# Kernel tuning notes

Hardware: AMD Instinct MI355X
Metric: run time of the kernel (lower is better)

Reference implementation:

```python
import jax, jax.numpy as jnp
import numpy as np

N_QUBITS = 8
N_LAYERS = 4
N_WIRES = N_QUBITS + 1  # circuit uses an extra ancilla wire
B = 16384
D = 512
LN_EPS = 1e-5


def _rx(theta):
    # RX(t) = [[cos(t/2), -i sin(t/2)], [-i sin(t/2), cos(t/2)]]; theta: () or (B,)
    c = jnp.cos(theta / 2).astype(jnp.complex64)
    s = (-1j) * jnp.sin(theta / 2).astype(jnp.complex64)
    return jnp.stack([jnp.stack([c, s], -1), jnp.stack([s, c], -1)], -2)


def _ry(theta):
    c = jnp.cos(theta / 2).astype(jnp.complex64)
    s = jnp.sin(theta / 2).astype(jnp.complex64)
    return jnp.stack([jnp.stack([c, -s], -1), jnp.stack([s, c], -1)], -2)


def _rz(theta):
    # RZ(t) = diag(e^{-it/2}, e^{it/2})
    half = (theta / 2).astype(jnp.complex64)
    em = jnp.exp(-1j * half)
    ep = jnp.exp(1j * half)
    z = jnp.zeros_like(em)
    return jnp.stack([jnp.stack([em, z], -1), jnp.stack([z, ep], -1)], -2)


def _apply_1q(state, U, wire):
    # state: (B,) + (2,)*N_WIRES ; U: (2,2) shared or (B,2,2) per-sample
    ax = 1 + wire
    s = jnp.moveaxis(state, ax, -1)
    if U.ndim == 2:
        s = jnp.einsum('ij,...j->...i', U, s)
    else:
        s = jnp.einsum('bij,b...j->b...i', U, s)
    return jnp.moveaxis(s, -1, ax)


def _cnot(state, c, t):
    # flip target wire t on the control=1 slice of wire c
    s = jnp.moveaxis(state, (1 + c, 1 + t), (-2, -1))
    s = jnp.stack([s[..., 0, :], jnp.flip(s[..., 1, :], axis=-1)], axis=-2)
    return jnp.moveaxis(s, (-2, -1), (1 + c, 1 + t))


def _quantum_circuit(angles, q_weights):
    # angles: (B, N_QUBITS) per-sample data angles; q_weights: (N_LAYERS, N_QUBITS+1)
    b = angles.shape[0]
    state = jnp.zeros((b, 2 ** N_WIRES), jnp.complex64).at[:, 0].set(1.0)
    state = state.reshape((b,) + (2,) * N_WIRES)
    # data encoding: RX, RZ with per-sample angles
    for i in range(N_QUBITS):
        state = _apply_1q(state, _rx(angles[:, i]), i)
        state = _apply_1q(state, _rz(angles[:, i]), i)
    # first variational layer
    for i in range(N_QUBITS):
        state = _apply_1q(state, _rx(q_weights[0, i]), i)
        state = _apply_1q(state, _rz(q_weights[1, i]), i)
    # entangling layers
    for l in range(1, N_LAYERS):
        for i in range(N_QUBITS):
            state = _cnot(state, i, (i + 1) % N_QUBITS)
            state = _apply_1q(state, _ry(q_weights[l, i]), i)
            state = _apply_1q(state, _rz(q_weights[l, i]), i)
        state = _cnot(state, N_QUBITS - 1, N_QUBITS)
        state = _apply_1q(state, _ry(q_weights[l, -1]), N_QUBITS)
    probs = state.real ** 2 + state.imag ** 2
    # <Z_i> = P(q_i=0) - P(q_i=1)
    zs = []
    for i in range(N_QUBITS):
        axes = tuple(1 + j for j in range(N_WIRES) if j != i)
        p = probs.sum(axes)  # (B, 2)
        zs.append(p[:, 0] - p[:, 1])
    return jnp.stack(zs, axis=1)  # (B, N_QUBITS)


def _forward(x, timestep, w_in, b_in, ln_gamma, ln_beta, q_weights, w_out, b_out):
    h = jnp.tanh(x @ w_in.T + b_in)  # (B, 8)
    mu = h.mean(-1, keepdims=True)
    var = ((h - mu) ** 2).mean(-1, keepdims=True)
    h = (h - mu) / jnp.sqrt(var + LN_EPS) * ln_gamma + ln_beta
    angles = h + timestep  # broadcast scalar timestep
    q_out = _quantum_circuit(angles, q_weights)
    out = q_out @ w_out.T + b_out
    return x + out  # input_dim == output_dim -> residual


def setup_inputs() -> dict:
    key = jax.random.key(0)
    ks = jax.random.split(key, 6)
    x = jax.random.normal(ks[0], (B, D), jnp.float32)
    timestep = jax.random.uniform(ks[1], (1,), jnp.float32)
    w_in = jax.random.normal(ks[2], (N_QUBITS, D), jnp.float32) * np.float32(1.0 / np.sqrt(D))
    b_in = jnp.zeros((N_QUBITS,), jnp.float32)
    ln_gamma = jnp.ones((N_QUBITS,), jnp.float32)
    ln_beta = jnp.zeros((N_QUBITS,), jnp.float32)
    q_weights = jax.random.uniform(ks[3], (N_LAYERS, N_QUBITS + 1), jnp.float32, 0.0, 2.0 * np.pi)
    w_out = jax.random.normal(ks[4], (D, N_QUBITS), jnp.float32) * np.float32(1.0 / np.sqrt(N_QUBITS))
    b_out = jnp.zeros((D,), jnp.float32)
    return {'x': x, 'timestep': timestep, 'w_in': w_in, 'b_in': b_in,
            'ln_gamma': ln_gamma, 'ln_beta': ln_beta, 'q_weights': q_weights,
            'w_out': w_out, 'b_out': b_out}


def reference(x, timestep, w_in, b_in, ln_gamma, ln_beta, q_weights, w_out, b_out):
    return _forward(x, timestep, w_in, b_in, ln_gamma, ln_beta, q_weights, w_out, b_out)
```

## Files before the change

### kernel.cpp

```cpp
#include <hip/hip_runtime.h>
#include <math.h>

#define NSAMP 16384
#define ND    512

typedef float f2 __attribute__((ext_vector_type(2)));
__device__ __forceinline__ f2 spl(float x) { return (f2){x, x}; }

template<int CTRL>
__device__ __forceinline__ float dppf(float x) {
  return __int_as_float(__builtin_amdgcn_update_dpp(
      __float_as_int(x), __float_as_int(x), CTRL, 0xF, 0xF, true));
}
template<int CTRL, int RM, int BM>
__device__ __forceinline__ float dppf_keep(float x) {
  return __int_as_float(__builtin_amdgcn_update_dpp(
      __float_as_int(x), __float_as_int(x), CTRL, RM, BM, false));
}
template<int P>
__device__ __forceinline__ float swzf(float x) {
  return __int_as_float(__builtin_amdgcn_ds_swizzle(__float_as_int(x), P));
}
__device__ __forceinline__ float bpermf(int addrB, float x) {
  return __int_as_float(__builtin_amdgcn_ds_bpermute(addrB, __float_as_int(x)));
}

#if __has_builtin(__builtin_amdgcn_permlane16_swap)
#define HAVE_PLSWAP 1
#endif
__device__ __forceinline__ void plswap16(float x, float& a, float& b) {
#ifdef HAVE_PLSWAP
  auto r = __builtin_amdgcn_permlane16_swap(__float_as_uint(x), __float_as_uint(x), false, false);
  a = __uint_as_float(r[0]); b = __uint_as_float(r[1]);
#else
  a = x; b = swzf<0x401F>(x);
#endif
}
__device__ __forceinline__ void plswap32(float x, float& a, float& b) {
#ifdef HAVE_PLSWAP
  auto r = __builtin_amdgcn_permlane32_swap(__float_as_uint(x), __float_as_uint(x), false, false);
  a = __uint_as_float(r[0]); b = __uint_as_float(r[1]);
#else
  a = x; b = __shfl_xor(x, 32, 64);
#endif
}

template<int M>
__device__ __forceinline__ f2 bfly2(f2 x) {
  f2 r;
  if constexpr (M == 1)       { r.x = dppf<0xB1>(x.x);    r.y = dppf<0xB1>(x.y); }
  else if constexpr (M == 2)  { r.x = dppf<0x4E>(x.x);    r.y = dppf<0x4E>(x.y); }
  else if constexpr (M == 8)  { r.x = dppf<0x128>(x.x);   r.y = dppf<0x128>(x.y); }
  else if constexpr (M == 4)  { r.x = swzf<0x101F>(x.x);  r.y = swzf<0x101F>(x.y); }
  else if constexpr (M == 16) { r.x = swzf<0x401F>(x.x);  r.y = swzf<0x401F>(x.y); }
  else                        { r.x = __shfl_xor(x.x, 32, 64); r.y = __shfl_xor(x.y, 32, 64); }
  return r;
}

__device__ __forceinline__ void fold8_allsum2(const float* yA, const float* yB,
                                              int lane, float& rA, float& rB) {
  float a4[4], b4[4];
#pragma unroll
  for (int i = 0; i < 4; ++i) {
    float kA = (lane & 1) ? yA[2 * i + 1] : yA[2 * i];
    float sA = (lane & 1) ? yA[2 * i]     : yA[2 * i + 1];
    float kB = (lane & 1) ? yB[2 * i + 1] : yB[2 * i];
    float sB = (lane & 1) ? yB[2 * i]     : yB[2 * i + 1];
    a4[i] = kA + dppf<0xB1>(sA);
    b4[i] = kB + dppf<0xB1>(sB);
  }
  float a2[2], b2[2];
#pragma unroll
  for (int i = 0; i < 2; ++i) {
    float kA = (lane & 2) ? a4[2 * i + 1] : a4[2 * i];
    float sA = (lane & 2) ? a4[2 * i]     : a4[2 * i + 1];
    float kB = (lane & 2) ? b4[2 * i + 1] : b4[2 * i];
    float sB = (lane & 2) ? b4[2 * i]     : b4[2 * i + 1];
    a2[i] = kA + dppf<0x4E>(sA);
    b2[i] = kB + dppf<0x4E>(sB);
  }
  float kA = (lane & 4) ? a2[1] : a2[0];
  float sA = (lane & 4) ? a2[0] : a2[1];
  float kB = (lane & 4) ? b2[1] : b2[0];
  float sB = (lane & 4) ? b2[0] : b2[1];
  rA = kA + swzf<0x101F>(sA);
  rB = kB + swzf<0x101F>(sB);
  rA += dppf<0x128>(rA);
  rB += dppf<0x128>(rB);
  { float a, b; plswap16(rA, a, b); rA = a + b; }
  { float a, b; plswap16(rB, a, b); rB = a + b; }
  { float a, b; plswap32(rA, a, b); rA = a + b; }
  { float a, b; plswap32(rB, a, b); rB = a + b; }
}

__device__ __forceinline__ float grp8_sum(float x) {
  x += dppf<0xB1>(x);
  x += dppf<0x4E>(x);
  x += swzf<0x101F>(x);
  return x;
}

__device__ __forceinline__ f2 cmul(f2 a, f2 b) {
  f2 bs = __builtin_shufflevector(b, b, 1, 0);
  f2 t  = (f2){-a.y, a.y} * bs;
  return spl(a.x) * b + t;
}

template<int LB>
__device__ __forceinline__ void ry_local(f2* s, float c, float sv) {
#pragma unroll
  for (int r0 = 0; r0 < 16; ++r0) {
    if ((r0 & 7) & (1 << LB)) continue;
    const int r1 = r0 | (1 << LB);
    f2 a0 = s[r0], a1 = s[r1];
    s[r0] = spl(c) * a0 - spl(sv) * a1;
    s[r1] = spl(sv) * a0 + spl(c) * a1;
  }
}
template<int LB>
__device__ __forceinline__ void rz_local(f2* s, f2 phm, f2 php) {
#pragma unroll
  for (int r = 0; r < 16; ++r) s[r] = cmul(s[r], ((r & 7) & (1 << LB)) ? php : phm);
}
template<int M>
__device__ __forceinline__ void ry_lane(f2* s, float c, float se) {
#pragma unroll
  for (int r = 0; r < 16; ++r) {
    f2 p = bfly2<M>(s[r]);
    s[r] = spl(c) * s[r] + spl(se) * p;
  }
}
template<int CB, int TB>
__device__ __forceinline__ void cnot_ll(f2* s) {
#pragma unroll
  for (int r0 = 0; r0 < 16; ++r0) {
    if (!((r0 & 7) & (1 << CB)) || ((r0 & 7) & (1 << TB))) continue;
    const int r1 = r0 | (1 << TB);
    f2 t = s[r0]; s[r0] = s[r1]; s[r1] = t;
  }
}
template<int CB, int TM>
__device__ __forceinline__ void cnot_lt(f2* s) {
#pragma unroll
  for (int r = 0; r < 16; ++r) {
    if (!((r & 7) & (1 << CB))) continue;
    s[r] = bfly2<TM>(s[r]);
  }
}
__device__ __forceinline__ void cnot_bperm(f2* s, int addrB) {
#pragma unroll
  for (int r = 0; r < 16; ++r) {
    s[r].x = bpermf(addrB, s[r].x);
    s[r].y = bpermf(addrB, s[r].y);
  }
}
__device__ __forceinline__ void cnot_m4_t1(f2* s) {
#pragma unroll
  for (int r = 0; r < 16; ++r) {
    s[r].x = dppf_keep<0xB1, 0xF, 0xA>(s[r].x);
    s[r].y = dppf_keep<0xB1, 0xF, 0xA>(s[r].y);
  }
}
__device__ __forceinline__ void cnot_m1_t2(f2* s) {
#pragma unroll
  for (int r = 0; r < 16; ++r) {
    s[r].x = dppf<0x6C>(s[r].x);
    s[r].y = dppf<0x6C>(s[r].y);
  }
}
template<int TB>
__device__ __forceinline__ void cnot_tl(f2* s, bool cc) {
#pragma unroll
  for (int r0 = 0; r0 < 16; ++r0) {
    if ((r0 & 7) & (1 << TB)) continue;
    const int r1 = r0 | (1 << TB);
    f2 n0, n1;
    n0.x = cc ? s[r1].x : s[r0].x;  n0.y = cc ? s[r1].y : s[r0].y;
    n1.x = cc ? s[r0].x : s[r1].x;  n1.y = cc ? s[r0].y : s[r1].y;
    s[r0] = n0; s[r1] = n1;
  }
}

__global__ void qpre_kernel(const float* __restrict__ qw, float* __restrict__ ws) {
  int t = threadIdx.x;
  if (t < 27) {
    float s, c; __sincosf(qw[9 + t] * 0.5f, &s, &c);
    ws[2 * t] = c; ws[2 * t + 1] = s;
  }
}

template<bool PRE>
struct Consts {
  const float* qw; const float* ws;
  __device__ __forceinline__ f2 ltrig(int l, int i) const {
    if constexpr (PRE) {
      return ((const f2*)ws)[(l - 1) * 9 + i];
    } else {
      float s, c; __sincosf(qw[l * 9 + i] * 0.5f, &s, &c);
      return (f2){c, s};
    }
  }
};

template<bool PRE, int MODE>
__device__ __forceinline__ void do_layer(f2* st, int lane, const Consts<PRE>& cst, int l,
                                         int addr56, int addr67, int addr78) {
  f2 t[9];
#pragma unroll
  for (int i = 0; i < 9; ++i) t[i] = cst.ltrig(l, i);

  cnot_ll<0, 1>(st);
  ry_local<0>(st, t[0].x, t[0].y);
  rz_local<0>(st, (f2){t[0].x, -t[0].y}, (f2){t[0].x, t[0].y});
  cnot_ll<1, 2>(st);
  ry_local<1>(st, t[1].x, t[1].y);
  cnot_lt<2, 4>(st);
  ry_local<2>(st, t[2].x, t[2].y);
  cnot_m4_t1(st);
  { float se = (lane & 4) ? t[3].y : -t[3].y;
    ry_lane<4>(st, t[3].x, se); }
  cnot_m1_t2(st);
  { float se = (lane & 1) ? t[4].y : -t[4].y;
    ry_lane<1>(st, t[4].x, se); }
  cnot_bperm(st, addr56);
  { float se = (lane & 2) ? t[5].y : -t[5].y;
    ry_lane<2>(st, t[5].x, se); }
  cnot_bperm(st, addr67);
  { float se = (lane & 8) ? t[6].y : -t[6].y;
    ry_lane<8>(st, t[6].x, se); }
  cnot_tl<0>(st, (lane & 16) != 0);
  { float se = (lane & 16) ? t[7].y : -t[7].y;
    ry_lane<16>(st, t[7].x, se); }

  if constexpr (MODE == 1) {
    const float wsel = (lane & 32) ? ((lane & 16) ? t[8].x : t[8].y)
                                   : ((lane & 16) ? -t[8].y : t[8].x);
#pragma unroll
    for (int r = 0; r < 16; ++r) st[r] = st[r] * spl(wsel);
  }
  if constexpr (MODE == 2) {
    cnot_bperm(st, addr78);
  }
  if constexpr (MODE != 3) {
    f2 L4[4];
#pragma unroll
    for (int k = 0; k < 4; ++k) {
      f2 p1 = (f2){t[1].x, (k & 1) ? t[1].y : -t[1].y};
      f2 p2 = (f2){t[2].x, (k & 2) ? t[2].y : -t[2].y};
      L4[k] = cmul(p1, p2);
    }
    f2 phW = (f2){t[3].x, (lane & 4)  ? t[3].y : -t[3].y};
    phW = cmul(phW, (f2){t[4].x, (lane & 1)  ? t[4].y : -t[4].y});
    phW = cmul(phW, (f2){t[5].x, (lane & 2)  ? t[5].y : -t[5].y});
    phW = cmul(phW, (f2){t[6].x, (lane & 8)  ? t[6].y : -t[6].y});
    phW = cmul(phW, (f2){t[7].x, (lane & 16) ? t[7].y : -t[7].y});
    f2 pr[4];
#pragma unroll
    for (int k = 0; k < 4; ++k) pr[k] = cmul(L4[k], phW);
#pragma unroll
    for (int r = 0; r < 16; ++r) st[r] = cmul(st[r], pr[((r & 7) >> 1) & 3]);
  }
}

template<bool PRE>
__global__ __launch_bounds__(256, 4) void qlayer_kernel(
    const float* __restrict__ x, const float* __restrict__ tstep,
    const float* __restrict__ w_in, const float* __restrict__ b_in,
    const float* __restrict__ g, const float* __restrict__ be,
    const float* __restrict__ qw, const float* __restrict__ w_out,
    const float* __restrict__ b_out, float* __restrict__ out,
    const float* __restrict__ ws)
{
  __shared__ __align__(16) float s_u[4][2][8][4];
  __shared__ __align__(16) float s_z[4][2][8];

  const int tid    = threadIdx.x;
  const int lane   = tid & 63;
  const int wv     = tid >> 6;
  const int smpA   = blockIdx.x * 8 + wv * 2;
  const int smpB   = smpA + 1;
  const int jq     = lane & 7;
  const int dbase  = lane << 3;

  const int addr56 = (lane ^ ((lane & 2) << 2)) << 2;
  const int addr67 = (lane ^ ((lane & 8) << 1)) << 2;
  const int addr78 = (lane ^ ((lane & 16) << 1)) << 2;

  const float4* xrA = (const float4*)(x + (size_t)smpA * ND + dbase);
  const float4* xrB = (const float4*)(x + (size_t)smpB * ND + dbase);
  const float4 xaA = xrA[0], xbA = xrA[1];
  const float4 xaB = xrB[0], xbB = xrB[1];
  const f2 a0 = (f2){xaA.x, xaA.y}, a1 = (f2){xaA.z, xaA.w};
  const f2 a2 = (f2){xbA.x, xbA.y}, a3 = (f2){xbA.z, xbA.w};
  const f2 b0 = (f2){xaB.x, xaB.y}, b1 = (f2){xaB.z, xaB.w};
  const f2 b2 = (f2){xbB.x, xbB.y}, b3 = (f2){xbB.z, xbB.w};

  float hA[8], hB[8];
#pragma unroll
  for (int j = 0; j < 8; ++j) {
    const float4* wj = (const float4*)(w_in + j * ND + dbase);
    float4 wa = wj[0], wb = wj[1];
    f2 w0 = (f2){wa.x, wa.y}, w1 = (f2){wa.z, wa.w};
    f2 w2 = (f2){wb.x, wb.y}, w3 = (f2){wb.z, wb.w};
    f2 accA = a0 * w0 + a1 * w1 + a2 * w2 + a3 * w3;
    f2 accB = b0 * w0 + b1 * w1 + b2 * w2 + b3 * w3;
    hA[j] = accA.x + accA.y;
    hB[j] = accB.x + accB.y;
  }
  float HA, HB;
  fold8_allsum2(hA, hB, lane, HA, HB);

  const float t0  = tstep[0];
  const float bj  = b_in[jq];
  const float gj  = g[jq];
  const float bej = be[jq];
  float tjA, tjB;
  {
    float vA = fminf(15.f, fmaxf(-15.f, HA + bj));
    float vB = fminf(15.f, fmaxf(-15.f, HB + bj));
    float eA = __expf(2.f * vA), eB = __expf(2.f * vB);
    tjA = (eA - 1.f) * __builtin_amdgcn_rcpf(eA + 1.f);
    tjB = (eB - 1.f) * __builtin_amdgcn_rcpf(eB + 1.f);
  }
  const float muA = grp8_sum(tjA) * 0.125f;
  const float muB = grp8_sum(tjB) * 0.125f;
  const float dvA = tjA - muA, dvB = tjB - muB;
  const float varA = grp8_sum(dvA * dvA) * 0.125f;
  const float varB = grp8_sum(dvB * dvB) * 0.125f;
  const float angA = dvA * rsqrtf(varA + 1e-5f) * gj + bej + t0;
  const float angB = dvB * rsqrtf(varB + 1e-5f) * gj + bej + t0;

  {
    float s0, c0, s1, c1;
    __sincosf(qw[jq] * 0.5f, &s0, &c0);
    __sincosf(qw[9 + jq] * 0.5f, &s1, &c1);
    f2 M00 = (f2){ c1 * c0, -s1 * c0};
    f2 M01 = (f2){-s1 * s0, -c1 * s0};
    f2 M10 = (f2){ s1 * s0, -c1 * s0};
    f2 M11 = (f2){ c1 * c0,  s1 * c0};
    float saA, caA; __sincosf(angA * 0.5f, &saA, &caA);
    float saB, caB; __sincosf(angB * 0.5f, &saB, &caB);
    f2 v0A = spl(caA) * (f2){caA, -saA};
    f2 v1A = spl(saA) * (f2){saA, -caA};
    f2 v0B = spl(caB) * (f2){caB, -saB};
    f2 v1B = spl(saB) * (f2){saB, -caB};
    f2 u0A = cmul(M00, v0A) + cmul(M01, v1A);
    f2 u1A = cmul(M10, v0A) + cmul(M11, v1A);
    f2 u0B = cmul(M00, v0B) + cmul(M01, v1B);
    f2 u1B = cmul(M10, v0B) + cmul(M11, v1B);
    if (lane < 16) {
      const int sb = lane >> 3;
      f2 u0 = sb ? u0B : u0A;
      f2 u1 = sb ? u1B : u1A;
      *(float4*)&s_u[wv][sb][jq][0] = (float4){u0.x, u0.y, u1.x, u1.y};
    }
  }
  asm volatile("s_waitcnt lgkmcnt(0)" ::: "memory");
  __builtin_amdgcn_sched_barrier(0);

  f2 st[16];
#pragma unroll
  for (int smp = 0; smp < 2; ++smp) {
    const f2* ub = (const f2*)&s_u[wv][smp][0][0];
    f2 r4 = ub[4 * 2 + ((lane >> 0) & 1)];
    f2 r5 = ub[5 * 2 + ((lane >> 1) & 1)];
    f2 r3 = ub[3 * 2 + ((lane >> 2) & 1)];
    f2 r6 = ub[6 * 2 + ((lane >> 3) & 1)];
    f2 r7 = ub[7 * 2 + ((lane >> 4) & 1)];
    f2 hl = cmul(cmul(cmul(cmul(r4, r5), r3), r6), r7);
    f2 u0q0 = ub[0], u1q0 = ub[1], u0q1 = ub[2], u1q1 = ub[3];
    f2 u0q2 = ub[4], u1q2 = ub[5];
    f2 t01[4];
#pragma unroll
    for (int q = 0; q < 4; ++q)
      t01[q] = cmul((q & 1) ? u1q0 : u0q0, (q & 2) ? u1q1 : u0q1);
#pragma unroll
    for (int r = 0; r < 8; ++r)
      st[smp * 8 + r] = cmul(cmul(t01[r & 3], (r & 4) ? u1q2 : u0q2), hl);
  }

  Consts<PRE> cst{qw, ws};
  do_layer<PRE, 1>(st, lane, cst, 1, addr56, addr67, addr78);
  do_layer<PRE, 2>(st, lane, cst, 2, addr56, addr67, addr78);
  do_layer<PRE, 3>(st, lane, cst, 3, addr56, addr67, addr78);

  float pA[8], pB[8];
#pragma unroll
  for (int r = 0; r < 8; ++r) {
    pA[r] = st[r].x * st[r].x + st[r].y * st[r].y;
    pB[r] = st[8 + r].x * st[8 + r].x + st[8 + r].y * st[8 + r].y;
  }
  float totA = 0.f, totB = 0.f;
#pragma unroll
  for (int r = 0; r < 8; ++r) { totA += pA[r]; totB += pB[r]; }

  float yA[8], yB[8];
  yA[0] = (pA[0] - pA[1]) + (pA[2] - pA[3]) + (pA[4] - pA[5]) + (pA[6] - pA[7]);
  yB[0] = (pB[0] - pB[1]) + (pB[2] - pB[3]) + (pB[4] - pB[5]) + (pB[6] - pB[7]);
  yA[1] = (pA[0] + pA[1]) - (pA[2] + pA[3]) + (pA[4] + pA[5]) - (pA[6] + pA[7]);
  yB[1] = (pB[0] + pB[1]) - (pB[2] + pB[3]) + (pB[4] + pB[5]) - (pB[6] + pB[7]);
  yA[2] = (pA[0] + pA[1] + pA[2] + pA[3]) - (pA[4] + pA[5] + pA[6] + pA[7]);
  yB[2] = (pB[0] + pB[1] + pB[2] + pB[3]) - (pB[4] + pB[5] + pB[6] + pB[7]);
  yA[3] = (lane & 4)  ? -totA : totA;  yB[3] = (lane & 4)  ? -totB : totB;
  yA[4] = (lane & 1)  ? -totA : totA;  yB[4] = (lane & 1)  ? -totB : totB;
  yA[5] = (lane & 2)  ? -totA : totA;  yB[5] = (lane & 2)  ? -totB : totB;
  yA[6] = (lane & 8)  ? -totA : totA;  yB[6] = (lane & 8)  ? -totB : totB;
  yA[7] = (lane & 16) ? -totA : totA;  yB[7] = (lane & 16) ? -totB : totB;
  float ZA, ZB;
  fold8_allsum2(yA, yB, lane, ZA, ZB);
  if (lane < 16) {
    const int sb = lane >> 3;
    s_z[wv][sb][jq] = sb ? ZB : ZA;
  }
  asm volatile("s_waitcnt lgkmcnt(0)" ::: "memory");
  __builtin_amdgcn_sched_barrier(0);

  const float4 zaA = *(const float4*)&s_z[wv][0][0];
  const float4 zbA = *(const float4*)&s_z[wv][0][4];
  const float4 zaB = *(const float4*)&s_z[wv][1][0];
  const float4 zbB = *(const float4*)&s_z[wv][1][4];

  const f2 zA01 = (f2){zaA.x, zaA.y}, zA23 = (f2){zaA.z, zaA.w};
  const f2 zA45 = (f2){zbA.x, zbA.y}, zA67 = (f2){zbA.z, zbA.w};
  const f2 zB01 = (f2){zaB.x, zaB.y}, zB23 = (f2){zaB.z, zaB.w};
  const f2 zB45 = (f2){zbB.x, zbB.y}, zB67 = (f2){zbB.z, zbB.w};
  const float4* wo = (const float4*)(w_out + (size_t)dbase * 8);
  const float4* bo = (const float4*)(b_out + dbase);
  const float4 bo0 = bo[0], bo1 = bo[1];
  const float xkA[8] = {xaA.x, xaA.y, xaA.z, xaA.w, xbA.x, xbA.y, xbA.z, xbA.w};
  const float xkB[8] = {xaB.x, xaB.y, xaB.z, xaB.w, xbB.x, xbB.y, xbB.z, xbB.w};
  const float bk[8]  = {bo0.x, bo0.y, bo0.z, bo0.w, bo1.x, bo1.y, bo1.z, bo1.w};
  float oA[8], oB[8];
#pragma unroll
  for (int k = 0; k < 8; ++k) {
    float4 wa = wo[2 * k];
    float4 wb = wo[2 * k + 1];
    f2 w01 = (f2){wa.x, wa.y}, w23 = (f2){wa.z, wa.w};
    f2 w45 = (f2){wb.x, wb.y}, w67 = (f2){wb.z, wb.w};
    f2 accA = zA01 * w01 + zA23 * w23 + zA45 * w45 + zA67 * w67;
    f2 accB = zB01 * w01 + zB23 * w23 + zB45 * w45 + zB67 * w67;
    oA[k] = xkA[k] + bk[k] + accA.x + accA.y;
    oB[k] = xkB[k] + bk[k] + accB.x + accB.y;
  }
  float4* outA = (float4*)(out + (size_t)smpA * ND + dbase);
  float4* outB = (float4*)(out + (size_t)smpB * ND + dbase);
  outA[0] = (float4){oA[0], oA[1], oA[2], oA[3]};
  outA[1] = (float4){oA[4], oA[5], oA[6], oA[7]};
  outB[0] = (float4){oB[0], oB[1], oB[2], oB[3]};
  outB[1] = (float4){oB[4], oB[5], oB[6], oB[7]};
}

extern "C" void kernel_launch(void* const* d_in, const int* in_sizes, int n_in,
                              void* d_out, int out_size, void* d_ws, size_t ws_size,
                              hipStream_t stream) {
  const float* x     = (const float*)d_in[0];
  const float* ts    = (const float*)d_in[1];
  const float* w_in  = (const float*)d_in[2];
  const float* b_in  = (const float*)d_in[3];
  const float* g     = (const float*)d_in[4];
  const float* be    = (const float*)d_in[5];
  const float* qw    = (const float*)d_in[6];
  const float* w_out = (const float*)d_in[7];
  const float* b_out = (const float*)d_in[8];
  float* out = (float*)d_out;

  const bool pre = (d_ws != nullptr) && (ws_size >= 256);
  if (pre) {
    qpre_kernel<<<dim3(1), dim3(64), 0, stream>>>(qw, (float*)d_ws);
    qlayer_kernel<true><<<dim3(NSAMP / 8), dim3(256), 0, stream>>>(
        x, ts, w_in, b_in, g, be, qw, w_out, b_out, out, (const float*)d_ws);
  } else {
    qlayer_kernel<false><<<dim3(NSAMP / 8), dim3(256), 0, stream>>>(
        x, ts, w_in, b_in, g, be, qw, w_out, b_out, out, (const float*)d_ws);
  }
}
```

Measured before the change: 56.54 us.

## Remap qubit 3 to lane bit 5 and replace bpermute CNOTs with DPP/swizzle

Changes the mapping of qubits to lane bits so qubit 3 sits on lane bit 5 instead of bit 4 (value 4). Several CNOTs that used ds_bpermute can then use DPP row-shuffles or swizzles with a per-lane select, and the 16/32-lane butterflies use permlane swaps with an XOR trick. The ancilla phase multiply is folded into the per-lane phase vector rather than applied to all 16 state registers. This is meant to cut LDS-crossbar permute traffic and ALU work in the circuit simulation, at the cost of extra selects and a tricky remapping that must stay consistent in the encoding and readout stages.

```diff
diff --git a/kernel.cpp b/kernel.cpp
--- a/kernel.cpp
+++ b/kernel.cpp
@@ -23,6 +23,9 @@
 }
 __device__ __forceinline__ float bpermf(int addrB, float x) {
   return __int_as_float(__builtin_amdgcn_ds_bpermute(addrB, __float_as_int(x)));
+}
+__device__ __forceinline__ float xor3f(float a, float b, float c) {
+  return __int_as_float(__float_as_int(a) ^ __float_as_int(b) ^ __float_as_int(c));
 }
 
 #if __has_builtin(__builtin_amdgcn_permlane16_swap)
@@ -44,16 +47,22 @@
   a = x; b = __shfl_xor(x, 32, 64);
 #endif
 }
+__device__ __forceinline__ float bf16v(float x) {
+  float a, b; plswap16(x, a, b); return xor3f(a, b, x);
+}
+__device__ __forceinline__ float bf32v(float x) {
+  float a, b; plswap32(x, a, b); return xor3f(a, b, x);
+}
 
 template<int M>
 __device__ __forceinline__ f2 bfly2(f2 x) {
   f2 r;
-  if constexpr (M == 1)       { r.x = dppf<0xB1>(x.x);    r.y = dppf<0xB1>(x.y); }
-  else if constexpr (M == 2)  { r.x = dppf<0x4E>(x.x);    r.y = dppf<0x4E>(x.y); }
-  else if constexpr (M == 8)  { r.x = dppf<0x128>(x.x);   r.y = dppf<0x128>(x.y); }
-  else if constexpr (M == 4)  { r.x = swzf<0x101F>(x.x);  r.y = swzf<0x101F>(x.y); }
-  else if constexpr (M == 16) { r.x = swzf<0x401F>(x.x);  r.y = swzf<0x401F>(x.y); }
-  else                        { r.x = __shfl_xor(x.x, 32, 64); r.y = __shfl_xor(x.y, 32, 64); }
+  if constexpr (M == 1)       { r.x = dppf<0xB1>(x.x);   r.y = dppf<0xB1>(x.y); }
+  else if constexpr (M == 2)  { r.x = dppf<0x4E>(x.x);   r.y = dppf<0x4E>(x.y); }
+  else if constexpr (M == 8)  { r.x = dppf<0x128>(x.x);  r.y = dppf<0x128>(x.y); }
+  else if constexpr (M == 4)  { r.x = swzf<0x101F>(x.x); r.y = swzf<0x101F>(x.y); }
+  else if constexpr (M == 16) { r.x = bf16v(x.x);        r.y = bf16v(x.y); }
+  else                        { r.x = bf32v(x.x);        r.y = bf32v(x.y); }
   return r;
 }
 
@@ -154,11 +163,11 @@
     s[r].y = bpermf(addrB, s[r].y);
   }
 }
-__device__ __forceinline__ void cnot_m4_t1(f2* s) {
-#pragma unroll
-  for (int r = 0; r < 16; ++r) {
-    s[r].x = dppf_keep<0xB1, 0xF, 0xA>(s[r].x);
-    s[r].y = dppf_keep<0xB1, 0xF, 0xA>(s[r].y);
+__device__ __forceinline__ void cnot_m32_t1(f2* s) {
+#pragma unroll
+  for (int r = 0; r < 16; ++r) {
+    s[r].x = dppf_keep<0xB1, 0xC, 0xF>(s[r].x);
+    s[r].y = dppf_keep<0xB1, 0xC, 0xF>(s[r].y);
   }
 }
 __device__ __forceinline__ void cnot_m1_t2(f2* s) {
@@ -166,6 +175,25 @@
   for (int r = 0; r < 16; ++r) {
     s[r].x = dppf<0x6C>(s[r].x);
     s[r].y = dppf<0x6C>(s[r].y);
+  }
+}
+template<int CTRL>
+__device__ __forceinline__ void cnot_cc_dpp(f2* s, bool cc) {
+#pragma unroll
+  for (int r = 0; r < 16; ++r) {
+    float px = dppf<CTRL>(s[r].x);
+    float py = dppf<CTRL>(s[r].y);
+    s[r].x = cc ? px : s[r].x;
+    s[r].y = cc ? py : s[r].y;
+  }
+}
+__device__ __forceinline__ void cnot_cc_swz4(f2* s, bool cc) {
+#pragma unroll
+  for (int r = 0; r < 16; ++r) {
+    float px = swzf<0x101F>(s[r].x);
+    float py = swzf<0x101F>(s[r].y);
+    s[r].x = cc ? px : s[r].x;
+    s[r].y = cc ? py : s[r].y;
   }
 }
 template<int TB>
@@ -204,7 +232,7 @@
 
 template<bool PRE, int MODE>
 __device__ __forceinline__ void do_layer(f2* st, int lane, const Consts<PRE>& cst, int l,
-                                         int addr56, int addr67, int addr78) {
+                                         int addr67) {
   f2 t[9];
 #pragma unroll
   for (int i = 0; i < 9; ++i) t[i] = cst.ltrig(l, i);
@@ -214,15 +242,15 @@
   rz_local<0>(st, (f2){t[0].x, -t[0].y}, (f2){t[0].x, t[0].y});
   cnot_ll<1, 2>(st);
   ry_local<1>(st, t[1].x, t[1].y);
-  cnot_lt<2, 4>(st);
+  cnot_lt<2, 32>(st);
   ry_local<2>(st, t[2].x, t[2].y);
-  cnot_m4_t1(st);
-  { float se = (lane & 4) ? t[3].y : -t[3].y;
-    ry_lane<4>(st, t[3].x, se); }
+  cnot_m32_t1(st);
+  { float se = (lane & 32) ? t[3].y : -t[3].y;
+    ry_lane<32>(st, t[3].x, se); }
   cnot_m1_t2(st);
   { float se = (lane & 1) ? t[4].y : -t[4].y;
     ry_lane<1>(st, t[4].x, se); }
-  cnot_bperm(st, addr56);
+  cnot_cc_dpp<0x128>(st, (lane & 2) != 0);
   { float se = (lane & 2) ? t[5].y : -t[5].y;
     ry_lane<2>(st, t[5].x, se); }
   cnot_bperm(st, addr67);
@@ -232,14 +260,8 @@
   { float se = (lane & 16) ? t[7].y : -t[7].y;
     ry_lane<16>(st, t[7].x, se); }
 
-  if constexpr (MODE == 1) {
-    const float wsel = (lane & 32) ? ((lane & 16) ? t[8].x : t[8].y)
-                                   : ((lane & 16) ? -t[8].y : t[8].x);
-#pragma unroll
-    for (int r = 0; r < 16; ++r) st[r] = st[r] * spl(wsel);
-  }
   if constexpr (MODE == 2) {
-    cnot_bperm(st, addr78);
+    cnot_cc_swz4(st, (lane & 16) != 0);
   }
   if constexpr (MODE != 3) {
     f2 L4[4];
@@ -249,11 +271,16 @@
       f2 p2 = (f2){t[2].x, (k & 2) ? t[2].y : -t[2].y};
       L4[k] = cmul(p1, p2);
     }
-    f2 phW = (f2){t[3].x, (lane & 4)  ? t[3].y : -t[3].y};
+    f2 phW = (f2){t[3].x, (lane & 32) ? t[3].y : -t[3].y};
     phW = cmul(phW, (f2){t[4].x, (lane & 1)  ? t[4].y : -t[4].y});
     phW = cmul(phW, (f2){t[5].x, (lane & 2)  ? t[5].y : -t[5].y});
     phW = cmul(phW, (f2){t[6].x, (lane & 8)  ? t[6].y : -t[6].y});
     phW = cmul(phW, (f2){t[7].x, (lane & 16) ? t[7].y : -t[7].y});
+    if constexpr (MODE == 1) {
+      const float wsel = (lane & 4) ? ((lane & 16) ? t[8].x : t[8].y)
+                                    : ((lane & 16) ? -t[8].y : t[8].x);
+      phW = phW * spl(wsel);
+    }
     f2 pr[4];
 #pragma unroll
     for (int k = 0; k < 4; ++k) pr[k] = cmul(L4[k], phW);
@@ -282,9 +309,7 @@
   const int jq     = lane & 7;
   const int dbase  = lane << 3;
 
-  const int addr56 = (lane ^ ((lane & 2) << 2)) << 2;
   const int addr67 = (lane ^ ((lane & 8) << 1)) << 2;
-  const int addr78 = (lane ^ ((lane & 16) << 1)) << 2;
 
   const float4* xrA = (const float4*)(x + (size_t)smpA * ND + dbase);
   const float4* xrB = (const float4*)(x + (size_t)smpB * ND + dbase);
@@ -364,9 +389,9 @@
     const f2* ub = (const f2*)&s_u[wv][smp][0][0];
     f2 r4 = ub[4 * 2 + ((lane >> 0) & 1)];
     f2 r5 = ub[5 * 2 + ((lane >> 1) & 1)];
-    f2 r3 = ub[3 * 2 + ((lane >> 2) & 1)];
     f2 r6 = ub[6 * 2 + ((lane >> 3) & 1)];
     f2 r7 = ub[7 * 2 + ((lane >> 4) & 1)];
+    f2 r3 = ub[3 * 2 + ((lane >> 5) & 1)];
     f2 hl = cmul(cmul(cmul(cmul(r4, r5), r3), r6), r7);
     f2 u0q0 = ub[0], u1q0 = ub[1], u0q1 = ub[2], u1q1 = ub[3];
     f2 u0q2 = ub[4], u1q2 = ub[5];
@@ -380,9 +405,9 @@
   }
 
   Consts<PRE> cst{qw, ws};
-  do_layer<PRE, 1>(st, lane, cst, 1, addr56, addr67, addr78);
-  do_layer<PRE, 2>(st, lane, cst, 2, addr56, addr67, addr78);
-  do_layer<PRE, 3>(st, lane, cst, 3, addr56, addr67, addr78);
+  do_layer<PRE, 1>(st, lane, cst, 1, addr67);
+  do_layer<PRE, 2>(st, lane, cst, 2, addr67);
+  do_layer<PRE, 3>(st, lane, cst, 3, addr67);
 
   float pA[8], pB[8];
 #pragma unroll
@@ -401,7 +426,7 @@
   yB[1] = (pB[0] + pB[1]) - (pB[2] + pB[3]) + (pB[4] + pB[5]) - (pB[6] + pB[7]);
   yA[2] = (pA[0] + pA[1] + pA[2] + pA[3]) - (pA[4] + pA[5] + pA[6] + pA[7]);
   yB[2] = (pB[0] + pB[1] + pB[2] + pB[3]) - (pB[4] + pB[5] + pB[6] + pB[7]);
-  yA[3] = (lane & 4)  ? -totA : totA;  yB[3] = (lane & 4)  ? -totB : totB;
+  yA[3] = (lane & 32) ? -totA : totA;  yB[3] = (lane & 32) ? -totB : totB;
   yA[4] = (lane & 1)  ? -totA : totA;  yB[4] = (lane & 1)  ? -totB : totB;
   yA[5] = (lane & 2)  ? -totA : totA;  yB[5] = (lane & 2)  ? -totB : totB;
   yA[6] = (lane & 8)  ? -totA : totA;  yB[6] = (lane & 8)  ? -totB : totB;
```

Measured after the change: 105.0 us. 1.86x slower.
